# Kernel tuning notes

Measured on AMD Instinct MI355X. Metric: run time of the kernel, lower is better.

Reference implementation:

```python
import jax, jax.numpy as jnp
import numpy as np

B, N, M, K = 8, 4096, 1024, 16   # clouds, points/cloud, fps samples/cloud (ratio=0.25), max neighbors
R = 0.3                          # radius
C_IN, H1, H2, C_OUT = 3, 64, 64, 128


def setup_inputs() -> dict:
    key = jax.random.key(0)
    ks = jax.random.split(key, 6)
    pos = jax.random.normal(ks[0], (B * N, 3), jnp.float32)
    x = jax.random.normal(ks[1], (B * N, C_IN), jnp.float32)
    batch = jnp.repeat(jnp.arange(B, dtype=jnp.int32), N)
    def lin(k, fan_in, fan_out):
        return jax.random.normal(k, (fan_in, fan_out), jnp.float32) / np.float32(np.sqrt(fan_in))
    W1 = lin(ks[2], C_IN + 3, H1); b1 = jnp.zeros((H1,), jnp.float32)
    W2 = lin(ks[3], H1, H2);       b2 = jnp.zeros((H2,), jnp.float32)
    W3 = lin(ks[4], H2, C_OUT);    b3 = jnp.zeros((C_OUT,), jnp.float32)
    return dict(x=x, pos=pos, batch=batch, W1=W1, b1=b1, W2=W2, b2=b2, W3=W3, b3=b3)


def _fps(pos_b):
    # farthest point sampling for one cloud: [N,3] -> [M] indices (start at point 0)
    d0 = jnp.sum((pos_b - pos_b[0]) ** 2, axis=-1)
    def body(d, _):
        i = jnp.argmax(d).astype(jnp.int32)
        d = jnp.minimum(d, jnp.sum((pos_b - pos_b[i]) ** 2, axis=-1))
        return d, i
    _, idxs = jax.lax.scan(body, d0, None, length=M - 1)
    return jnp.concatenate([jnp.zeros((1,), jnp.int32), idxs])


def _radius(pos_s_b, pos_b):
    # for each of M query points, first-K (by index) points within R: -> neigh [M,K], mask [M,K]
    d2 = jnp.sum((pos_s_b[:, None, :] - pos_b[None, :, :]) ** 2, axis=-1)  # [M,N]
    valid = d2 <= R * R
    keyed = jnp.where(valid, jnp.arange(N, dtype=jnp.int32)[None, :], N)
    first = jnp.sort(keyed, axis=1)[:, :K]
    mask = first < N
    return jnp.where(mask, first, 0), mask


def reference(x, pos, batch, W1, b1, W2, b2, W3, b3):
    posB = pos.reshape(B, N, 3)
    xB = x.reshape(B, N, C_IN)

    idx = jax.vmap(_fps)(posB)                                       # [B,M]
    pos_s = jnp.take_along_axis(posB, idx[..., None], axis=1)        # [B,M,3]

    neigh, mask = jax.vmap(_radius)(pos_s, posB)                     # [B,M,K]

    # flat (global) indices, matching PyG's concatenated-batch indexing
    src_flat = jnp.arange(B, dtype=jnp.int32)[:, None, None] * N + neigh            # [B,M,K]
    dst_flat = jnp.arange(B, dtype=jnp.int32)[:, None] * M + jnp.arange(M, dtype=jnp.int32)[None, :]  # [B,M]
    # PointConv(add_self_loops=True): remove_self_loops on numeric equality, then add (i,i)
    mask = mask & (src_flat != dst_flat[..., None])

    gather = jax.vmap(lambda a, nb: a[nb])
    x_j = gather(xB, neigh)                                          # [B,M,K,C_IN]
    pos_j = gather(posB, neigh)                                      # [B,M,K,3]
    rel = pos_j - pos_s[:, :, None, :]

    # self-loop edges: source point index i == target index i in flat indexing
    i_self = dst_flat.reshape(-1)                                    # [B*M]
    x_self = x[i_self]                                               # [B*M,C_IN]
    rel_self = pos[i_self] - pos_s.reshape(-1, 3)

    f_rad = jnp.concatenate([x_j, rel], axis=-1)                     # [B,M,K,6]
    f_self = jnp.concatenate([x_self, rel_self], axis=-1).reshape(B, M, 1, C_IN + 3)
    feats = jnp.concatenate([f_rad, f_self], axis=2)                 # [B,M,K+1,6]
    m_all = jnp.concatenate([mask, jnp.ones((B, M, 1), bool)], axis=2)

    h = jax.nn.relu(feats @ W1 + b1)
    h = jax.nn.relu(h @ W2 + b2)
    h = h @ W3 + b3                                                  # [B,M,K+1,C_OUT]
    h = jnp.where(m_all[..., None], h, -jnp.inf)
    out = jnp.max(h, axis=2).reshape(B * M, C_OUT)                   # max aggregation

    batch_s = jnp.repeat(jnp.arange(B, dtype=batch.dtype), M)
    return out, pos_s.reshape(B * M, 3), batch_s
```

## Files before the change

### kernel.cpp

```cpp
#include <hip/hip_runtime.h>
#include <hip/hip_bf16.h>
#include <math.h>

constexpr int BB   = 8;
constexpr int NN   = 4096;
constexpr int MM   = 1024;
constexpr int KK   = 16;
constexpr int COUT = 128;
constexpr int NWRK = 992;
#define RSQ 0.09f

__device__ __forceinline__ float dist2_exact(float ax, float ay, float az,
                                             float bx, float by, float bz) {
    float dx = __fsub_rn(ax, bx);
    float dy = __fsub_rn(ay, by);
    float dz = __fsub_rn(az, bz);
    return __fadd_rn(__fadd_rn(__fmul_rn(dx, dx), __fmul_rn(dy, dy)), __fmul_rn(dz, dz));
}

template<int CTRL>
__device__ __forceinline__ unsigned dpp_mov_u(unsigned v) {
    return (unsigned)__builtin_amdgcn_update_dpp((int)v, (int)v, CTRL, 0xF, 0xF, false);
}
template<int CTRL, int RMASK>
__device__ __forceinline__ unsigned dpp_mov_rm(unsigned v) {
    return (unsigned)__builtin_amdgcn_update_dpp((int)v, (int)v, CTRL, RMASK, 0xF, false);
}
__device__ __forceinline__ float readlane_f(float v, int j) {
    return __int_as_float(__builtin_amdgcn_readlane(__float_as_int(v), j));
}
__device__ __forceinline__ unsigned umax2(unsigned a, unsigned b) { return a > b ? a : b; }
__device__ __forceinline__ unsigned umin2(unsigned a, unsigned b) { return a < b ? a : b; }

__global__ __launch_bounds__(256, 1) void fused_kernel(const float* __restrict__ x,
                                                       const float* __restrict__ pos,
                                                       const float* __restrict__ W1,
                                                       const float* __restrict__ b1,
                                                       const float* __restrict__ W2,
                                                       const float* __restrict__ b2,
                                                       const float* __restrict__ W3,
                                                       const float* __restrict__ b3,
                                                       unsigned* __restrict__ gsel,
                                                       float* __restrict__ out,
                                                       float* __restrict__ pos_s,
                                                       float* __restrict__ batch_s) {
    __shared__ float4 spos[NN];
    __shared__ int    shist[MM];
    __shared__ __align__(16) unsigned long long slotK[2][4];
    __shared__ float sW2[64 * 64];
    __shared__ float sW3[64 * 128];
    __shared__ int   nslot[4][16];

    const int tid  = threadIdx.x;
    const int lane = tid & 63;
    const int wave = tid >> 6;

    if (blockIdx.x < BB) {
        const int b = blockIdx.x;
        const float* pb = pos + (size_t)b * NN * 3;

        for (int i = tid; i < NN; i += 256)
            spos[i] = make_float4(pb[i * 3 + 0], pb[i * 3 + 1], pb[i * 3 + 2], 0.0f);
        for (int i = tid; i < MM; i += 256)
            batch_s[(size_t)b * MM + i] = (float)b;
        if (tid == 0) {
            shist[0] = 0;
            __hip_atomic_store(&gsel[(size_t)b * MM], 1u, __ATOMIC_RELAXED,
                               __HIP_MEMORY_SCOPE_AGENT);
        }
        if (tid < 8) slotK[tid >> 2][tid & 3] = 0ull;
        __syncthreads();

        float px[16], py[16], pz[16], d[16];
        const float4 p0 = spos[0];
#pragma unroll
        for (int k = 0; k < 16; k++) {
            float4 pt = spos[tid + k * 256];
            px[k] = pt.x; py[k] = pt.y; pz[k] = pt.z;
            d[k] = dist2_exact(pt.x, pt.y, pt.z, p0.x, p0.y, p0.z);
        }
        float bv;
        {
            float t1[8], t2[4];
#pragma unroll
            for (int k = 0; k < 8; k++) t1[k] = fmaxf(d[2 * k], d[2 * k + 1]);
#pragma unroll
            for (int k = 0; k < 4; k++) t2[k] = fmaxf(t1[2 * k], t1[2 * k + 1]);
            bv = fmaxf(fmaxf(t2[0], t2[1]), fmaxf(t2[2], t2[3]));
        }

        for (int m = 1; m < MM; m++) {
            const int par = m & 1;
            const unsigned tagm = (unsigned)m;

            const unsigned bvb = __float_as_uint(bv);

            unsigned rv = bvb;
            rv = umax2(rv, dpp_mov_u<0x111>(rv));
            rv = umax2(rv, dpp_mov_u<0x112>(rv));
            rv = umax2(rv, dpp_mov_u<0x114>(rv));
            rv = umax2(rv, dpp_mov_u<0x118>(rv));
            rv = umax2(rv, dpp_mov_rm<0x142, 0xa>(rv));
            rv = umax2(rv, dpp_mov_rm<0x143, 0xc>(rv));
            const unsigned vstar = (unsigned)__builtin_amdgcn_readlane((int)rv, 63);

            unsigned kmask = 0u;
#pragma unroll
            for (int k = 0; k < 16; k++)
                kmask |= (d[k] == bv) ? (1u << k) : 0u;
            const unsigned bi = (unsigned)(tid + (__builtin_ctz(kmask) << 8));

            unsigned cand = (bvb == vstar) ? bi : 0xFFFFFFFFu;
            cand = umin2(cand, dpp_mov_u<0x111>(cand));
            cand = umin2(cand, dpp_mov_u<0x112>(cand));
            cand = umin2(cand, dpp_mov_u<0x114>(cand));
            cand = umin2(cand, dpp_mov_u<0x118>(cand));
            cand = umin2(cand, dpp_mov_rm<0x142, 0xa>(cand));
            cand = umin2(cand, dpp_mov_rm<0x143, 0xc>(cand));

            if (lane == 63) {
                slotK[par][wave] =
                    ((unsigned long long)vstar << 32)
                    | (unsigned long long)(((4095u - cand) << 10) | tagm);
            }
            __syncthreads();

            const ulonglong2 ka = *(const ulonglong2*)&slotK[par][0];
            const ulonglong2 kb = *(const ulonglong2*)&slotK[par][2];
            const unsigned long long kA = (ka.x > ka.y) ? ka.x : ka.y;
            const unsigned long long kB = (kb.x > kb.y) ? kb.x : kb.y;
            const unsigned long long kk = (kA > kB) ? kA : kB;
            const int fi = 4095 - (int)(((unsigned)kk >> 10) & 4095u);

            const float4 sp = spos[fi];

            if (tid == 0) shist[m] = fi;
            if (((m & 7) == 1) && m > 1 && tid < 8) {
                const int base = m - 8;
                __hip_atomic_store(&gsel[(size_t)b * MM + base + tid],
                                   (unsigned)(shist[base + tid] + 1),
                                   __ATOMIC_RELAXED, __HIP_MEMORY_SCOPE_AGENT);
            }

            if (m < MM - 1) {
#pragma unroll
                for (int k = 0; k < 16; k++) {
                    float nd = dist2_exact(px[k], py[k], pz[k], sp.x, sp.y, sp.z);
                    d[k] = fminf(d[k], nd);
                }
                float t1[8], t2[4];
#pragma unroll
                for (int k = 0; k < 8; k++) t1[k] = fmaxf(d[2 * k], d[2 * k + 1]);
#pragma unroll
                for (int k = 0; k < 4; k++) t2[k] = fmaxf(t1[2 * k], t1[2 * k + 1]);
                bv = fmaxf(fmaxf(t2[0], t2[1]), fmaxf(t2[2], t2[3]));
            }
        }

        __syncthreads();
        if (tid < 7) {
            const int mm = 1017 + tid;
            __hip_atomic_store(&gsel[(size_t)b * MM + mm],
                               (unsigned)(shist[mm] + 1),
                               __ATOMIC_RELAXED, __HIP_MEMORY_SCOPE_AGENT);
        }
        for (int i = tid; i < MM; i += 256) {
            float4 sp = spos[shist[i]];
            size_t o = (size_t)b * MM + i;
            pos_s[o * 3 + 0] = sp.x;
            pos_s[o * 3 + 1] = sp.y;
            pos_s[o * 3 + 2] = sp.z;
        }
        return;
    }

    {
        const float4* s2 = (const float4*)W2;
        float4*       d2 = (float4*)sW2;
        for (int i = tid; i < 64 * 64 / 4; i += 256) d2[i] = s2[i];
        const float4* s3 = (const float4*)W3;
        float4*       d3 = (float4*)sW3;
        for (int i = tid; i < 64 * 128 / 4; i += 256) d3[i] = s3[i];
    }
    float w1c[6];
#pragma unroll
    for (int c = 0; c < 6; c++) w1c[c] = W1[c * 64 + lane];
    const float bb1  = b1[lane];
    const float bb2  = b2[lane];
    const float bb3a = b3[lane];
    const float bb3b = b3[64 + lane];
    __syncthreads();

    const int W = (blockIdx.x - BB) * 4 + wave;

    int myq[9]; int nq = 0;
#pragma unroll
    for (int k = 0; k < 9; k++) {
        int q = W + NWRK * k;
        if (q < BB * MM) myq[nq++] = q;
    }
    for (int i = 1; i < nq; i++) {
        int v = myq[i]; int j = i - 1;
        while (j >= 0 && (myq[j] & 1023) > (v & 1023)) { myq[j + 1] = myq[j]; j--; }
        myq[j + 1] = v;
    }

    for (int i = 0; i < nq; i++) {
        const int q = myq[i];

        unsigned v = 0u;
        int guard = 0;
        for (;;) {
            v = __hip_atomic_load(&gsel[q], __ATOMIC_RELAXED,
                                  __HIP_MEMORY_SCOPE_AGENT);
            if (v >= 1u && v <= (unsigned)NN) break;
            if (++guard > 6000) break;
            __builtin_amdgcn_s_sleep(127);
        }
        if (v == 0u || v > (unsigned)NN) continue;

        const int b  = q >> 10;
        const int fi = (int)v - 1;
        const float qx = pos[((size_t)b * NN + fi) * 3 + 0];
        const float qy = pos[((size_t)b * NN + fi) * 3 + 1];
        const float qz = pos[((size_t)b * NN + fi) * 3 + 2];

        if (lane < 16) nslot[wave][lane] = 0;
        const float* pb = pos + (size_t)b * NN * 3;
        int cnt = 0;
        for (int c = 0; c < NN / 64; c++) {
            int p = c * 64 + lane;
            float px = pb[p * 3 + 0], py = pb[p * 3 + 1], pz = pb[p * 3 + 2];
            float d2 = dist2_exact(qx, qy, qz, px, py, pz);
            bool val = (d2 <= RSQ);
            unsigned long long msk = __ballot(val);
            if (val) {
                int rank = __popcll(msk & ((1ull << lane) - 1ull));
                int slot = cnt + rank;
                if (slot < KK) nslot[wave][slot] = p;
            }
            cnt += __popcll(msk);
            if (cnt >= KK) break;
        }
        const int cnt16 = min(cnt, KK);

        const int4 n0 = *(const int4*)&nslot[wave][0];
        const int4 n1 = *(const int4*)&nslot[wave][4];
        const int4 n2 = *(const int4*)&nslot[wave][8];
        const int4 n3 = *(const int4*)&nslot[wave][12];
        const int nidx[16] = { n0.x, n0.y, n0.z, n0.w, n1.x, n1.y, n1.z, n1.w,
                               n2.x, n2.y, n2.z, n2.w, n3.x, n3.y, n3.z, n3.w };

        float h[17];
        unsigned vmask = 1u << 16;
#pragma unroll
        for (int e = 0; e < 16; e++) {
            const int p = (e < cnt16) ? nidx[e] : 0;
            const int g = b * NN + p;
            if ((e < cnt16) && (g != q)) vmask |= (1u << e);
            const float f0 = x[(size_t)g * 3 + 0];
            const float f1 = x[(size_t)g * 3 + 1];
            const float f2 = x[(size_t)g * 3 + 2];
            const float f3 = pos[(size_t)g * 3 + 0] - qx;
            const float f4 = pos[(size_t)g * 3 + 1] - qy;
            const float f5 = pos[(size_t)g * 3 + 2] - qz;
            float t = bb1 + f0 * w1c[0] + f1 * w1c[1] + f2 * w1c[2]
                          + f3 * w1c[3] + f4 * w1c[4] + f5 * w1c[5];
            h[e] = fmaxf(t, 0.0f);
        }
        {
            const int g = q;
            const float f0 = x[(size_t)g * 3 + 0];
            const float f1 = x[(size_t)g * 3 + 1];
            const float f2 = x[(size_t)g * 3 + 2];
            const float f3 = pos[(size_t)g * 3 + 0] - qx;
            const float f4 = pos[(size_t)g * 3 + 1] - qy;
            const float f5 = pos[(size_t)g * 3 + 2] - qz;
            float t = bb1 + f0 * w1c[0] + f1 * w1c[1] + f2 * w1c[2]
                          + f3 * w1c[3] + f4 * w1c[4] + f5 * w1c[5];
            h[16] = fmaxf(t, 0.0f);
        }

        float acc[17];
#pragma unroll
        for (int e = 0; e < 17; e++) acc[e] = bb2;
#pragma unroll 2
        for (int j = 0; j < 64; j++) {
            const float wj = sW2[j * 64 + lane];
#pragma unroll
            for (int e = 0; e < 17; e++) {
                const float hj = readlane_f(h[e], j);
                acc[e] = __builtin_fmaf(hj, wj, acc[e]);
            }
        }
#pragma unroll
        for (int e = 0; e < 17; e++) h[e] = fmaxf(acc[e], 0.0f);

        float a0[17], a1[17];
#pragma unroll
        for (int e = 0; e < 17; e++) { a0[e] = bb3a; a1[e] = bb3b; }
#pragma unroll 2
        for (int j = 0; j < 64; j++) {
            const float wa = sW3[j * 128 + lane];
            const float wb = sW3[j * 128 + 64 + lane];
#pragma unroll
            for (int e = 0; e < 17; e++) {
                const float hj = readlane_f(h[e], j);
                a0[e] = __builtin_fmaf(hj, wa, a0[e]);
                a1[e] = __builtin_fmaf(hj, wb, a1[e]);
            }
        }

        float m0 = -INFINITY, m1 = -INFINITY;
#pragma unroll
        for (int e = 0; e < 17; e++) {
            const bool vv = (vmask >> e) & 1u;
            m0 = vv ? fmaxf(m0, a0[e]) : m0;
            m1 = vv ? fmaxf(m1, a1[e]) : m1;
        }
        out[(size_t)q * COUT + lane]      = m0;
        out[(size_t)q * COUT + 64 + lane] = m1;
    }
}

extern "C" void kernel_launch(void* const* d_in, const int* in_sizes, int n_in,
                              void* d_out, int out_size, void* d_ws, size_t ws_size,
                              hipStream_t stream) {
    const float* x   = (const float*)d_in[0];
    const float* pos = (const float*)d_in[1];
    const float* W1 = (const float*)d_in[3];
    const float* b1 = (const float*)d_in[4];
    const float* W2 = (const float*)d_in[5];
    const float* b2 = (const float*)d_in[6];
    const float* W3 = (const float*)d_in[7];
    const float* b3 = (const float*)d_in[8];

    float* outF    = (float*)d_out;
    float* out     = outF;
    float* pos_s   = outF + (size_t)BB * MM * COUT;
    float* batch_s = pos_s + (size_t)BB * MM * 3;

    unsigned* gsel = (unsigned*)d_ws;

    hipMemsetAsync(gsel, 0, (size_t)BB * MM * sizeof(unsigned), stream);

    fused_kernel<<<256, 256, 0, stream>>>(x, pos, W1, b1, W2, b2, W3, b3,
                                          gsel, out, pos_s, batch_s);
}
```

Before: 805.0 us.

## Double block size to 512 threads and use packed FP32 math in FPS

```diff
diff --git a/kernel.cpp b/kernel.cpp
--- a/kernel.cpp
+++ b/kernel.cpp
@@ -7,8 +7,12 @@
 constexpr int MM   = 1024;
 constexpr int KK   = 16;
 constexpr int COUT = 128;
-constexpr int NWRK = 992;
+constexpr int TPB  = 512;
+constexpr int WPB  = 8;
+constexpr int NWRK = 1984;
 #define RSQ 0.09f
+
+typedef float f32x2 __attribute__((ext_vector_type(2)));
 
 __device__ __forceinline__ float dist2_exact(float ax, float ay, float az,
                                              float bx, float by, float bz) {
@@ -31,8 +35,22 @@
 }
 __device__ __forceinline__ unsigned umax2(unsigned a, unsigned b) { return a > b ? a : b; }
 __device__ __forceinline__ unsigned umin2(unsigned a, unsigned b) { return a < b ? a : b; }
-
-__global__ __launch_bounds__(256, 1) void fused_kernel(const float* __restrict__ x,
+__device__ __forceinline__ unsigned long long umax64(unsigned long long a, unsigned long long b) {
+    return a > b ? a : b;
+}
+
+__device__ __forceinline__ f32x2 pk_add(f32x2 a, f32x2 b) {
+    f32x2 r;
+    asm("v_pk_add_f32 %0, %1, %2" : "=v"(r) : "v"(a), "v"(b));
+    return r;
+}
+__device__ __forceinline__ f32x2 pk_mul(f32x2 a, f32x2 b) {
+    f32x2 r;
+    asm("v_pk_mul_f32 %0, %1, %2" : "=v"(r) : "v"(a), "v"(b));
+    return r;
+}
+
+__global__ __launch_bounds__(512, 1) void fused_kernel(const float* __restrict__ x,
                                                        const float* __restrict__ pos,
                                                        const float* __restrict__ W1,
                                                        const float* __restrict__ b1,
@@ -46,10 +64,10 @@
                                                        float* __restrict__ batch_s) {
     __shared__ float4 spos[NN];
     __shared__ int    shist[MM];
-    __shared__ __align__(16) unsigned long long slotK[2][4];
+    __shared__ __align__(16) unsigned long long slotK[2][WPB];
     __shared__ float sW2[64 * 64];
     __shared__ float sW3[64 * 128];
-    __shared__ int   nslot[4][16];
+    __shared__ int   nslot[WPB][16];
 
     const int tid  = threadIdx.x;
     const int lane = tid & 63;
@@ -59,34 +77,37 @@
         const int b = blockIdx.x;
         const float* pb = pos + (size_t)b * NN * 3;
 
-        for (int i = tid; i < NN; i += 256)
+        for (int i = tid; i < NN; i += TPB)
             spos[i] = make_float4(pb[i * 3 + 0], pb[i * 3 + 1], pb[i * 3 + 2], 0.0f);
-        for (int i = tid; i < MM; i += 256)
+        for (int i = tid; i < MM; i += TPB)
             batch_s[(size_t)b * MM + i] = (float)b;
         if (tid == 0) {
             shist[0] = 0;
             __hip_atomic_store(&gsel[(size_t)b * MM], 1u, __ATOMIC_RELAXED,
                                __HIP_MEMORY_SCOPE_AGENT);
         }
-        if (tid < 8) slotK[tid >> 2][tid & 3] = 0ull;
+        if (tid < 2 * WPB) slotK[tid >> 3][tid & 7] = 0ull;
         __syncthreads();
 
-        float px[16], py[16], pz[16], d[16];
+        f32x2 px2[4], py2[4], pz2[4];
+        float d[8];
         const float4 p0 = spos[0];
 #pragma unroll
-        for (int k = 0; k < 16; k++) {
-            float4 pt = spos[tid + k * 256];
-            px[k] = pt.x; py[k] = pt.y; pz[k] = pt.z;
-            d[k] = dist2_exact(pt.x, pt.y, pt.z, p0.x, p0.y, p0.z);
+        for (int p = 0; p < 4; p++) {
+            float4 a = spos[tid + (2 * p) * TPB];
+            float4 c = spos[tid + (2 * p + 1) * TPB];
+            px2[p][0] = a.x; px2[p][1] = c.x;
+            py2[p][0] = a.y; py2[p][1] = c.y;
+            pz2[p][0] = a.z; pz2[p][1] = c.z;
+            d[2 * p]     = dist2_exact(a.x, a.y, a.z, p0.x, p0.y, p0.z);
+            d[2 * p + 1] = dist2_exact(c.x, c.y, c.z, p0.x, p0.y, p0.z);
         }
         float bv;
         {
-            float t1[8], t2[4];
-#pragma unroll
-            for (int k = 0; k < 8; k++) t1[k] = fmaxf(d[2 * k], d[2 * k + 1]);
-#pragma unroll
-            for (int k = 0; k < 4; k++) t2[k] = fmaxf(t1[2 * k], t1[2 * k + 1]);
-            bv = fmaxf(fmaxf(t2[0], t2[1]), fmaxf(t2[2], t2[3]));
+            float t1[4];
+#pragma unroll
+            for (int k = 0; k < 4; k++) t1[k] = fmaxf(d[2 * k], d[2 * k + 1]);
+            bv = fmaxf(fmaxf(t1[0], t1[1]), fmaxf(t1[2], t1[3]));
         }
 
         for (int m = 1; m < MM; m++) {
@@ -106,9 +127,9 @@
 
             unsigned kmask = 0u;
 #pragma unroll
-            for (int k = 0; k < 16; k++)
+            for (int k = 0; k < 8; k++)
                 kmask |= (d[k] == bv) ? (1u << k) : 0u;
-            const unsigned bi = (unsigned)(tid + (__builtin_ctz(kmask) << 8));
+            const unsigned bi = (unsigned)(tid + (__builtin_ctz(kmask) << 9));
 
             unsigned cand = (bvb == vstar) ? bi : 0xFFFFFFFFu;
             cand = umin2(cand, dpp_mov_u<0x111>(cand));
@@ -127,9 +148,11 @@
 
             const ulonglong2 ka = *(const ulonglong2*)&slotK[par][0];
             const ulonglong2 kb = *(const ulonglong2*)&slotK[par][2];
-            const unsigned long long kA = (ka.x > ka.y) ? ka.x : ka.y;
-            const unsigned long long kB = (kb.x > kb.y) ? kb.x : kb.y;
-            const unsigned long long kk = (kA > kB) ? kA : kB;
+            const ulonglong2 kc = *(const ulonglong2*)&slotK[par][4];
+            const ulonglong2 kd = *(const ulonglong2*)&slotK[par][6];
+            const unsigned long long kA = umax64(umax64(ka.x, ka.y), umax64(kb.x, kb.y));
+            const unsigned long long kB = umax64(umax64(kc.x, kc.y), umax64(kd.x, kd.y));
+            const unsigned long long kk = umax64(kA, kB);
             const int fi = 4095 - (int)(((unsigned)kk >> 10) & 4095u);
 
             const float4 sp = spos[fi];
@@ -143,17 +166,26 @@
             }
 
             if (m < MM - 1) {
-#pragma unroll
-                for (int k = 0; k < 16; k++) {
-                    float nd = dist2_exact(px[k], py[k], pz[k], sp.x, sp.y, sp.z);
-                    d[k] = fminf(d[k], nd);
+                const f32x2 nsx = { -sp.x, -sp.x };
+                const f32x2 nsy = { -sp.y, -sp.y };
+                const f32x2 nsz = { -sp.z, -sp.z };
+#pragma unroll
+                for (int p = 0; p < 4; p++) {
+                    f32x2 dx = pk_add(px2[p], nsx);
+                    f32x2 dy = pk_add(py2[p], nsy);
+                    f32x2 dz = pk_add(pz2[p], nsz);
+                    f32x2 xx = pk_mul(dx, dx);
+                    f32x2 yy = pk_mul(dy, dy);
+                    f32x2 zz = pk_mul(dz, dz);
+                    f32x2 ss = pk_add(xx, yy);
+                    f32x2 tt = pk_add(ss, zz);
+                    d[2 * p]     = fminf(d[2 * p],     tt[0]);
+                    d[2 * p + 1] = fminf(d[2 * p + 1], tt[1]);
                 }
-                float t1[8], t2[4];
-#pragma unroll
-                for (int k = 0; k < 8; k++) t1[k] = fmaxf(d[2 * k], d[2 * k + 1]);
-#pragma unroll
-                for (int k = 0; k < 4; k++) t2[k] = fmaxf(t1[2 * k], t1[2 * k + 1]);
-                bv = fmaxf(fmaxf(t2[0], t2[1]), fmaxf(t2[2], t2[3]));
+                float t1[4];
+#pragma unroll
+                for (int k = 0; k < 4; k++) t1[k] = fmaxf(d[2 * k], d[2 * k + 1]);
+                bv = fmaxf(fmaxf(t1[0], t1[1]), fmaxf(t1[2], t1[3]));
             }
         }
 
@@ -164,7 +196,7 @@
                                (unsigned)(shist[mm] + 1),
                                __ATOMIC_RELAXED, __HIP_MEMORY_SCOPE_AGENT);
         }
-        for (int i = tid; i < MM; i += 256) {
+        for (int i = tid; i < MM; i += TPB) {
             float4 sp = spos[shist[i]];
             size_t o = (size_t)b * MM + i;
             pos_s[o * 3 + 0] = sp.x;
@@ -177,10 +209,10 @@
     {
         const float4* s2 = (const float4*)W2;
         float4*       d2 = (float4*)sW2;
-        for (int i = tid; i < 64 * 64 / 4; i += 256) d2[i] = s2[i];
+        for (int i = tid; i < 64 * 64 / 4; i += TPB) d2[i] = s2[i];
         const float4* s3 = (const float4*)W3;
         float4*       d3 = (float4*)sW3;
-        for (int i = tid; i < 64 * 128 / 4; i += 256) d3[i] = s3[i];
+        for (int i = tid; i < 64 * 128 / 4; i += TPB) d3[i] = s3[i];
     }
     float w1c[6];
 #pragma unroll
@@ -191,11 +223,11 @@
     const float bb3b = b3[64 + lane];
     __syncthreads();
 
-    const int W = (blockIdx.x - BB) * 4 + wave;
-
-    int myq[9]; int nq = 0;
-#pragma unroll
-    for (int k = 0; k < 9; k++) {
+    const int W = (blockIdx.x - BB) * WPB + wave;
+
+    int myq[5]; int nq = 0;
+#pragma unroll
+    for (int k = 0; k < 5; k++) {
         int q = W + NWRK * k;
         if (q < BB * MM) myq[nq++] = q;
     }
@@ -344,6 +376,6 @@
 
     hipMemsetAsync(gsel, 0, (size_t)BB * MM * sizeof(unsigned), stream);
 
-    fused_kernel<<<256, 256, 0, stream>>>(x, pos, W1, b1, W2, b2, W3, b3,
+    fused_kernel<<<256, TPB, 0, stream>>>(x, pos, W1, b1, W2, b2, W3, b3,
                                           gsel, out, pos_s, batch_s);
 }
```

Result: slower. 848.2 us (+5.4%).

## Pack FPS distances into float2 vectors and use ballot-based argmax in waves

Applied to the files above, without the earlier changes.

```diff
diff --git a/kernel.cpp b/kernel.cpp
--- a/kernel.cpp
+++ b/kernel.cpp
@@ -10,6 +10,8 @@
 constexpr int NWRK = 992;
 #define RSQ 0.09f
 
+typedef float f32x2 __attribute__((ext_vector_type(2)));
+
 __device__ __forceinline__ float dist2_exact(float ax, float ay, float az,
                                              float bx, float by, float bz) {
     float dx = __fsub_rn(ax, bx);
@@ -30,7 +32,9 @@
     return __int_as_float(__builtin_amdgcn_readlane(__float_as_int(v), j));
 }
 __device__ __forceinline__ unsigned umax2(unsigned a, unsigned b) { return a > b ? a : b; }
-__device__ __forceinline__ unsigned umin2(unsigned a, unsigned b) { return a < b ? a : b; }
+__device__ __forceinline__ unsigned long long umax64(unsigned long long a, unsigned long long b) {
+    return a > b ? a : b;
+}
 
 __global__ __launch_bounds__(256, 1) void fused_kernel(const float* __restrict__ x,
                                                        const float* __restrict__ pos,
@@ -71,19 +75,23 @@
         if (tid < 8) slotK[tid >> 2][tid & 3] = 0ull;
         __syncthreads();
 
-        float px[16], py[16], pz[16], d[16];
+        f32x2 px2[8], py2[8], pz2[8], d2[8];
         const float4 p0 = spos[0];
 #pragma unroll
-        for (int k = 0; k < 16; k++) {
-            float4 pt = spos[tid + k * 256];
-            px[k] = pt.x; py[k] = pt.y; pz[k] = pt.z;
-            d[k] = dist2_exact(pt.x, pt.y, pt.z, p0.x, p0.y, p0.z);
+        for (int p = 0; p < 8; p++) {
+            float4 a = spos[tid * 16 + 2 * p];
+            float4 c = spos[tid * 16 + 2 * p + 1];
+            px2[p][0] = a.x; px2[p][1] = c.x;
+            py2[p][0] = a.y; py2[p][1] = c.y;
+            pz2[p][0] = a.z; pz2[p][1] = c.z;
+            d2[p][0] = dist2_exact(a.x, a.y, a.z, p0.x, p0.y, p0.z);
+            d2[p][1] = dist2_exact(c.x, c.y, c.z, p0.x, p0.y, p0.z);
         }
         float bv;
         {
             float t1[8], t2[4];
 #pragma unroll
-            for (int k = 0; k < 8; k++) t1[k] = fmaxf(d[2 * k], d[2 * k + 1]);
+            for (int p = 0; p < 8; p++) t1[p] = fmaxf(d2[p][0], d2[p][1]);
 #pragma unroll
             for (int k = 0; k < 4; k++) t2[k] = fmaxf(t1[2 * k], t1[2 * k + 1]);
             bv = fmaxf(fmaxf(t2[0], t2[1]), fmaxf(t2[2], t2[3]));
@@ -106,30 +114,29 @@
 
             unsigned kmask = 0u;
 #pragma unroll
-            for (int k = 0; k < 16; k++)
-                kmask |= (d[k] == bv) ? (1u << k) : 0u;
-            const unsigned bi = (unsigned)(tid + (__builtin_ctz(kmask) << 8));
-
-            unsigned cand = (bvb == vstar) ? bi : 0xFFFFFFFFu;
-            cand = umin2(cand, dpp_mov_u<0x111>(cand));
-            cand = umin2(cand, dpp_mov_u<0x112>(cand));
-            cand = umin2(cand, dpp_mov_u<0x114>(cand));
-            cand = umin2(cand, dpp_mov_u<0x118>(cand));
-            cand = umin2(cand, dpp_mov_rm<0x142, 0xa>(cand));
-            cand = umin2(cand, dpp_mov_rm<0x143, 0xc>(cand));
-
-            if (lane == 63) {
+            for (int p = 0; p < 8; p++) {
+                kmask |= (d2[p][0] == bv) ? (1u << (2 * p)) : 0u;
+                kmask |= (d2[p][1] == bv) ? (1u << (2 * p + 1)) : 0u;
+            }
+            const int kstar = __builtin_ctz(kmask);
+
+            const unsigned long long ball = __ballot(bvb == vstar);
+            const int L  = (int)__builtin_ctzll(ball);
+            const int kL = __builtin_amdgcn_readlane(kstar, L);
+            const unsigned g = ((unsigned)(wave * 64 + L) << 4) | (unsigned)kL;
+
+            if (lane == 0) {
                 slotK[par][wave] =
                     ((unsigned long long)vstar << 32)
-                    | (unsigned long long)(((4095u - cand) << 10) | tagm);
+                    | (unsigned long long)(((4095u - g) << 10) | tagm);
             }
             __syncthreads();
 
             const ulonglong2 ka = *(const ulonglong2*)&slotK[par][0];
             const ulonglong2 kb = *(const ulonglong2*)&slotK[par][2];
-            const unsigned long long kA = (ka.x > ka.y) ? ka.x : ka.y;
-            const unsigned long long kB = (kb.x > kb.y) ? kb.x : kb.y;
-            const unsigned long long kk = (kA > kB) ? kA : kB;
+            const unsigned long long kA = umax64(ka.x, ka.y);
+            const unsigned long long kB = umax64(kb.x, kb.y);
+            const unsigned long long kk = umax64(kA, kB);
             const int fi = 4095 - (int)(((unsigned)kk >> 10) & 4095u);
 
             const float4 sp = spos[fi];
@@ -143,14 +150,22 @@
             }
 
             if (m < MM - 1) {
-#pragma unroll
-                for (int k = 0; k < 16; k++) {
-                    float nd = dist2_exact(px[k], py[k], pz[k], sp.x, sp.y, sp.z);
-                    d[k] = fminf(d[k], nd);
+#pragma clang fp contract(off)
+                const f32x2 sx = { sp.x, sp.x };
+                const f32x2 sy = { sp.y, sp.y };
+                const f32x2 sz = { sp.z, sp.z };
+#pragma unroll
+                for (int p = 0; p < 8; p++) {
+                    f32x2 dx = px2[p] - sx;
+                    f32x2 dy = py2[p] - sy;
+                    f32x2 dz = pz2[p] - sz;
+                    f32x2 tt = dx * dx + dy * dy + dz * dz;
+                    d2[p][0] = fminf(d2[p][0], tt[0]);
+                    d2[p][1] = fminf(d2[p][1], tt[1]);
                 }
                 float t1[8], t2[4];
 #pragma unroll
-                for (int k = 0; k < 8; k++) t1[k] = fmaxf(d[2 * k], d[2 * k + 1]);
+                for (int p = 0; p < 8; p++) t1[p] = fmaxf(d2[p][0], d2[p][1]);
 #pragma unroll
                 for (int k = 0; k < 4; k++) t2[k] = fmaxf(t1[2 * k], t1[2 * k + 1]);
                 bv = fmaxf(fmaxf(t2[0], t2[1]), fmaxf(t2[2], t2[3]));
```

Result: faster. 749.4 us (-6.9%).
